# Kernel tuning notes

Measured on AMD Instinct MI355X. Metric: run time of the kernel, lower is better.

## Reference

```python
import jax, jax.numpy as jnp
import numpy as np

B, N, E, H, FF = 8, 1024, 512, 8, 2048
D = E // H
SCALE = D ** -0.5
EPS = 1e-5


def _layernorm(x, g, b):
    mu = jnp.mean(x, axis=-1, keepdims=True)
    var = jnp.mean((x - mu) ** 2, axis=-1, keepdims=True)
    return (x - mu) * jax.lax.rsqrt(var + EPS) * g + b


def setup_inputs() -> dict:
    key = jax.random.key(0)
    ks = jax.random.split(key, 16)
    s = lambda fan_in: 1.0 / np.sqrt(fan_in)
    inp = {"x": jax.random.normal(ks[0], (B, N, E), jnp.float32)}
    # attention projections, stored as [in, out] so y = x @ W + b
    inp["Wq"] = jax.random.uniform(ks[1], (E, E), jnp.float32, -s(E), s(E))
    inp["bq"] = jnp.zeros((E,), jnp.float32)
    inp["Wk"] = jax.random.uniform(ks[2], (E, E), jnp.float32, -s(E), s(E))
    inp["bk"] = jnp.zeros((E,), jnp.float32)
    inp["Wv"] = jax.random.uniform(ks[3], (E, E), jnp.float32, -s(E), s(E))
    inp["bv"] = jnp.zeros((E,), jnp.float32)
    inp["Wo"] = jax.random.uniform(ks[4], (E, E), jnp.float32, -s(E), s(E))
    inp["bo"] = jnp.zeros((E,), jnp.float32)
    # layernorms
    inp["g1"] = jnp.ones((E,), jnp.float32)
    inp["b1"] = jnp.zeros((E,), jnp.float32)
    inp["g2"] = jnp.ones((E,), jnp.float32)
    inp["b2"] = jnp.zeros((E,), jnp.float32)
    # feed-forward
    inp["W1"] = jax.random.uniform(ks[5], (E, FF), jnp.float32, -s(E), s(E))
    inp["bf1"] = jnp.zeros((FF,), jnp.float32)
    inp["W2"] = jax.random.uniform(ks[6], (FF, E), jnp.float32, -s(FF), s(FF))
    inp["bf2"] = jnp.zeros((E,), jnp.float32)
    return inp


def reference(x, Wq, bq, Wk, bk, Wv, bv, Wo, bo, g1, b1, g2, b2, W1, bf1, W2, bf2):
    # --- multi-head self-attention (equivalent to the edge scatter-softmax:
    # softmax over all source nodes j for each target node i) ---
    q = (x @ Wq + bq).reshape(B, N, H, D)
    k = (x @ Wk + bk).reshape(B, N, H, D)
    v = (x @ Wv + bv).reshape(B, N, H, D)
    scores = jnp.einsum("bnhd,bmhd->bhnm", q, k) * SCALE  # [B,H,N,N]
    attn = jax.nn.softmax(scores, axis=-1)
    ctx = jnp.einsum("bhnm,bmhd->bnhd", attn, v).reshape(B, N, E)
    attn_out = ctx @ Wo + bo
    # --- residual + norm1 ---
    h1 = _layernorm(x + attn_out, g1, b1)
    # --- FFN: linear -> relu -> linear ---
    ffn = jax.nn.relu(h1 @ W1 + bf1) @ W2 + bf2
    # --- residual + norm2 ---
    return _layernorm(h1 + ffn, g2, b2)
```

## Files before the change

### kernel.cpp

```cpp
#include <hip/hip_runtime.h>
#include <cstdint>
#include <cstddef>

typedef unsigned short u16;
typedef __attribute__((ext_vector_type(8))) short bf16x8;
typedef __attribute__((ext_vector_type(4))) float f32x4;
typedef __attribute__((ext_vector_type(16))) float f32x16;

#define EPI_F32 0
#define EPI_BF16_RELU 1
#define EPI_QKV 2

#define QSCALE 0.18033688011112042f

__device__ __forceinline__ u16 f2bf(float f) {
  uint32_t u = __float_as_uint(f);
  return (u16)((u + 0x7FFFu + ((u >> 16) & 1u)) >> 16);
}

__device__ __forceinline__ uint32_t cvt_pk_bf16(float lo, float hi) {
  uint32_t r;
  asm("v_cvt_pk_bf16_f32 %0, %1, %2" : "=v"(r) : "v"(lo), "v"(hi));
  return r;
}

__device__ __forceinline__ float fexp2(float x) { return __builtin_amdgcn_exp2f(x); }

__device__ __forceinline__ void gload_lds16(const void* g, void* l) {
  __builtin_amdgcn_global_load_lds((const __attribute__((address_space(1))) void*)g,
                                   (__attribute__((address_space(3))) void*)l, 16, 0, 0);
}

__global__ __launch_bounds__(256) void cvt_kernel(const float* __restrict__ in,
                                                  u16* __restrict__ out, int n8) {
  const int i = blockIdx.x * 256 + threadIdx.x;
  if (i >= n8) return;
  const float4* p = (const float4*)in + (size_t)i * 2;
  float4 a = p[0], b = p[1];
  union { u16 u[8]; uint4 q; } pk;
  pk.u[0] = f2bf(a.x); pk.u[1] = f2bf(a.y); pk.u[2] = f2bf(a.z); pk.u[3] = f2bf(a.w);
  pk.u[4] = f2bf(b.x); pk.u[5] = f2bf(b.y); pk.u[6] = f2bf(b.z); pk.u[7] = f2bf(b.w);
  ((uint4*)out)[i] = pk.q;
}

__global__ __launch_bounds__(256) void tcvt_kernel(const float* __restrict__ W,
                                                   u16* __restrict__ Wt, int K, int N) {
  __shared__ float tl[32][33];
  const int t = threadIdx.x;
  const int kr0 = blockIdx.y * 32, nc0 = blockIdx.x * 32;
  const int r = t >> 3, cq = (t & 7) * 4;
  float4 v = *(const float4*)&W[(size_t)(kr0 + r) * N + nc0 + cq];
  tl[r][cq + 0] = v.x; tl[r][cq + 1] = v.y; tl[r][cq + 2] = v.z; tl[r][cq + 3] = v.w;
  __syncthreads();
  union { u16 u[4]; uint2 q; } pk;
#pragma unroll
  for (int j = 0; j < 4; ++j) pk.u[j] = f2bf(tl[cq + j][r]);
  *(uint2*)&Wt[(size_t)(nc0 + r) * K + kr0 + cq] = pk.q;
}

__global__ __launch_bounds__(256) void packb_kernel(const float* __restrict__ bq,
                                                    const float* __restrict__ bk,
                                                    const float* __restrict__ bv,
                                                    float* __restrict__ out) {
  const int i = blockIdx.x * 256 + threadIdx.x;
  if (i >= 1536) return;
  out[i] = i < 512 ? bq[i] : (i < 1024 ? bk[i - 512] : bv[i - 1024]);
}

template<int BM, int BN, int WM, int WN, int EPI>
__global__ __launch_bounds__(256) void gemm_kernel(
    const u16* __restrict__ A, const u16* __restrict__ Bt,
    const float* __restrict__ bias, void* __restrict__ out,
    int M, int N, int K) {
  constexpr int NWN = BN / WN;
  constexpr int MI = WM / 16, NI = WN / 16;
  __shared__ u16 As[BM * 32];
  __shared__ u16 Bs[BN * 32];
  const int tid = threadIdx.x;
  const int lane = tid & 63;
  const int wave = tid >> 6;
  const int m0 = blockIdx.y * BM;
  const int n0 = blockIdx.x * BN;
  const int wm = wave / NWN, wn = wave % NWN;
  const int g = lane >> 4, lr = lane & 15;
  const int srow = lane >> 2, scol = (lane & 3) * 8;

  f32x4 acc[MI][NI] = {};

  for (int k0 = 0; k0 < K; k0 += 32) {
#pragma unroll
    for (int ch = wave; ch < BM / 16; ch += 4)
      gload_lds16(A + (size_t)(m0 + ch * 16 + srow) * K + k0 + scol, &As[ch * 512]);
#pragma unroll
    for (int ch = wave; ch < BN / 16; ch += 4)
      gload_lds16(Bt + (size_t)(n0 + ch * 16 + srow) * K + k0 + scol, &Bs[ch * 512]);
    __syncthreads();
    bf16x8 a[MI], b[NI];
#pragma unroll
    for (int mi = 0; mi < MI; ++mi) a[mi] = *(const bf16x8*)&As[(wm * WM + mi * 16 + lr) * 32 + g * 8];
#pragma unroll
    for (int ni = 0; ni < NI; ++ni) b[ni] = *(const bf16x8*)&Bs[(wn * WN + ni * 16 + lr) * 32 + g * 8];
#pragma unroll
    for (int mi = 0; mi < MI; ++mi)
#pragma unroll
      for (int ni = 0; ni < NI; ++ni)
        acc[mi][ni] = __builtin_amdgcn_mfma_f32_16x16x32_bf16(a[mi], b[ni], acc[mi][ni], 0, 0, 0);
    __syncthreads();
  }

#pragma unroll
  for (int mi = 0; mi < MI; ++mi) {
#pragma unroll
    for (int ni = 0; ni < NI; ++ni) {
      const int col = n0 + wn * WN + ni * 16 + lr;
      const float bv = bias[col];
      f32x4 v = acc[mi][ni];
#pragma unroll
      for (int r = 0; r < 4; ++r) {
        const int row = m0 + wm * WM + mi * 16 + g * 4 + r;
        const float y = v[r] + bv;
        if (EPI == EPI_F32) {
          ((float*)out)[(size_t)row * N + col] = y;
        } else if (EPI == EPI_BF16_RELU) {
          ((u16*)out)[(size_t)row * N + col] = f2bf(fmaxf(y, 0.f));
        } else {
          u16* qb = (u16*)out;
          const int sec = col >> 9, cs = col & 511;
          const int b = row >> 10, t = row & 1023, h = cs >> 6, d = cs & 63;
          if (sec == 0)
            qb[((size_t)((b * 8 + h) * 1024 + t)) * 64 + d] = f2bf(y * QSCALE);
          else if (sec == 1)
            qb[4194304 + ((size_t)((b * 8 + h) * 1024 + t)) * 64 + d] = f2bf(y);
          else
            qb[8388608 + ((size_t)((b * 8 + h) * 64 + d)) * 1024 + t] = f2bf(y);
        }
      }
    }
  }
}

__global__ __launch_bounds__(256, 2) void attn3_kernel(
    const u16* __restrict__ Q, const u16* __restrict__ K,
    const u16* __restrict__ Vt, u16* __restrict__ ctx) {
  __shared__ u16 tl[4 * 2048];
  const int tid = threadIdx.x, lane = tid & 63, w = tid >> 6;
  const int bh = blockIdx.x >> 3, qb = blockIdx.x & 7;
  const int c = lane & 31, g = lane >> 5;
  const int q0 = qb * 128 + w * 32;

  const u16* Qp = Q + ((size_t)bh * 1024 + q0 + c) * 64 + g * 8;
  const bf16x8 qf0 = *(const bf16x8*)(Qp);
  const bf16x8 qf1 = *(const bf16x8*)(Qp + 16);
  const bf16x8 qf2 = *(const bf16x8*)(Qp + 32);
  const bf16x8 qf3 = *(const bf16x8*)(Qp + 48);

  const u16* Kbase = K + (size_t)bh * 65536;
  const u16* Vbase = Vt + (size_t)bh * 65536;

  f32x16 cacc[2] = {};
  float mrun = -1e30f, lrun = 0.f;

  const u16* Kp0 = Kbase + (size_t)c * 64 + g * 8;
  bf16x8 kf0 = *(const bf16x8*)(Kp0);
  bf16x8 kf1 = *(const bf16x8*)(Kp0 + 16);
  bf16x8 kf2 = *(const bf16x8*)(Kp0 + 32);
  bf16x8 kf3 = *(const bf16x8*)(Kp0 + 48);
  bf16x8 kf4 = *(const bf16x8*)(Kp0 + 2048);
  bf16x8 kf5 = *(const bf16x8*)(Kp0 + 2048 + 16);
  bf16x8 kf6 = *(const bf16x8*)(Kp0 + 2048 + 32);
  bf16x8 kf7 = *(const bf16x8*)(Kp0 + 2048 + 48);

  for (int kt = 0; kt < 16; ++kt) {
    const int key0 = kt * 64;
    const int keyn = ((kt + 1) & 15) * 64;
    const u16* Vp = Vbase + (size_t)c * 1024 + key0 + g * 8;
    const bf16x8 va00 = *(const bf16x8*)(Vp);
    const bf16x8 va01 = *(const bf16x8*)(Vp + 16);
    const bf16x8 va10 = *(const bf16x8*)(Vp + 32768);
    const bf16x8 va11 = *(const bf16x8*)(Vp + 32768 + 16);
    const bf16x8 vb00 = *(const bf16x8*)(Vp + 32);
    const bf16x8 vb01 = *(const bf16x8*)(Vp + 48);
    const bf16x8 vb10 = *(const bf16x8*)(Vp + 32768 + 32);
    const bf16x8 vb11 = *(const bf16x8*)(Vp + 32768 + 48);
    const u16* Kpn = Kbase + (size_t)(keyn + c) * 64 + g * 8;
    const bf16x8 n0 = *(const bf16x8*)(Kpn);
    const bf16x8 n1 = *(const bf16x8*)(Kpn + 16);
    const bf16x8 n2 = *(const bf16x8*)(Kpn + 32);
    const bf16x8 n3 = *(const bf16x8*)(Kpn + 48);
    const bf16x8 n4 = *(const bf16x8*)(Kpn + 2048);
    const bf16x8 n5 = *(const bf16x8*)(Kpn + 2048 + 16);
    const bf16x8 n6 = *(const bf16x8*)(Kpn + 2048 + 32);
    const bf16x8 n7 = *(const bf16x8*)(Kpn + 2048 + 48);

    f32x16 sa = {}, sb = {};
    sa = __builtin_amdgcn_mfma_f32_32x32x16_bf16(kf0, qf0, sa, 0, 0, 0);
    sb = __builtin_amdgcn_mfma_f32_32x32x16_bf16(kf4, qf0, sb, 0, 0, 0);
    sa = __builtin_amdgcn_mfma_f32_32x32x16_bf16(kf1, qf1, sa, 0, 0, 0);
    sb = __builtin_amdgcn_mfma_f32_32x32x16_bf16(kf5, qf1, sb, 0, 0, 0);
    sa = __builtin_amdgcn_mfma_f32_32x32x16_bf16(kf2, qf2, sa, 0, 0, 0);
    sb = __builtin_amdgcn_mfma_f32_32x32x16_bf16(kf6, qf2, sb, 0, 0, 0);
    sa = __builtin_amdgcn_mfma_f32_32x32x16_bf16(kf3, qf3, sa, 0, 0, 0);
    sb = __builtin_amdgcn_mfma_f32_32x32x16_bf16(kf7, qf3, sb, 0, 0, 0);

    float tm[16];
#pragma unroll
    for (int r = 0; r < 16; ++r) tm[r] = fmaxf(sa[r], sb[r]);
#pragma unroll
    for (int st = 8; st >= 1; st >>= 1)
#pragma unroll
      for (int r = 0; r < st; ++r) tm[r] = fmaxf(tm[r], tm[r + st]);
    const float mt = fmaxf(tm[0], __shfl_xor(tm[0], 32));
    if (!__all(mt <= mrun)) {
      const float mnew = fmaxf(mrun, mt);
      const float al = fexp2(mrun - mnew);
#pragma unroll
      for (int r = 0; r < 16; ++r) { cacc[0][r] *= al; cacc[1][r] *= al; }
      lrun *= al;
      mrun = mnew;
    }
    float pa[16], pb[16];
#pragma unroll
    for (int r = 0; r < 16; ++r) pa[r] = fexp2(sa[r] - mrun);
#pragma unroll
    for (int r = 0; r < 16; ++r) pb[r] = fexp2(sb[r] - mrun);
    float ts[16];
#pragma unroll
    for (int r = 0; r < 16; ++r) ts[r] = pa[r] + pb[r];
#pragma unroll
    for (int st = 8; st >= 1; st >>= 1)
#pragma unroll
      for (int r = 0; r < st; ++r) ts[r] += ts[r + st];
    lrun += ts[0] + __shfl_xor(ts[0], 32);

    uint32_t wda[8], pwa[8], wdb[8], pwb[8];
#pragma unroll
    for (int i = 0; i < 8; ++i) wda[i] = cvt_pk_bf16(pa[2 * i], pa[2 * i + 1]);
#pragma unroll
    for (int i = 0; i < 8; ++i) wdb[i] = cvt_pk_bf16(pb[2 * i], pb[2 * i + 1]);
#pragma unroll
    for (int i = 0; i < 8; ++i) pwa[i] = __shfl_xor((int)wda[i], 32);
#pragma unroll
    for (int i = 0; i < 8; ++i) pwb[i] = __shfl_xor((int)wdb[i], 32);
    union { uint32_t u[4]; bf16x8 v; } b0a, b1a, b0b, b1b;
    const bool glo = (g == 0);
    b0a.u[0] = glo ? wda[0] : pwa[2]; b0a.u[1] = glo ? wda[1] : pwa[3];
    b0a.u[2] = glo ? pwa[0] : wda[2]; b0a.u[3] = glo ? pwa[1] : wda[3];
    b1a.u[0] = glo ? wda[4] : pwa[6]; b1a.u[1] = glo ? wda[5] : pwa[7];
    b1a.u[2] = glo ? pwa[4] : wda[6]; b1a.u[3] = glo ? pwa[5] : wda[7];
    b0b.u[0] = glo ? wdb[0] : pwb[2]; b0b.u[1] = glo ? wdb[1] : pwb[3];
    b0b.u[2] = glo ? pwb[0] : wdb[2]; b0b.u[3] = glo ? pwb[1] : wdb[3];
    b1b.u[0] = glo ? wdb[4] : pwb[6]; b1b.u[1] = glo ? wdb[5] : pwb[7];
    b1b.u[2] = glo ? pwb[4] : wdb[6]; b1b.u[3] = glo ? pwb[5] : wdb[7];

    cacc[0] = __builtin_amdgcn_mfma_f32_32x32x16_bf16(va00, b0a.v, cacc[0], 0, 0, 0);
    cacc[1] = __builtin_amdgcn_mfma_f32_32x32x16_bf16(va10, b0a.v, cacc[1], 0, 0, 0);
    cacc[0] = __builtin_amdgcn_mfma_f32_32x32x16_bf16(va01, b1a.v, cacc[0], 0, 0, 0);
    cacc[1] = __builtin_amdgcn_mfma_f32_32x32x16_bf16(va11, b1a.v, cacc[1], 0, 0, 0);
    cacc[0] = __builtin_amdgcn_mfma_f32_32x32x16_bf16(vb00, b0b.v, cacc[0], 0, 0, 0);
    cacc[1] = __builtin_amdgcn_mfma_f32_32x32x16_bf16(vb10, b0b.v, cacc[1], 0, 0, 0);
    cacc[0] = __builtin_amdgcn_mfma_f32_32x32x16_bf16(vb01, b1b.v, cacc[0], 0, 0, 0);
    cacc[1] = __builtin_amdgcn_mfma_f32_32x32x16_bf16(vb11, b1b.v, cacc[1], 0, 0, 0);

    kf0 = n0; kf1 = n1; kf2 = n2; kf3 = n3;
    kf4 = n4; kf5 = n5; kf6 = n6; kf7 = n7;
  }

  const float inv = 1.0f / lrun;
  u16* tw = &tl[w * 2048];
#pragma unroll
  for (int h2 = 0; h2 < 2; ++h2) {
#pragma unroll
    for (int rq = 0; rq < 4; ++rq) {
      const u16 x0 = f2bf(cacc[h2][4 * rq + 0] * inv);
      const u16 x1 = f2bf(cacc[h2][4 * rq + 1] * inv);
      const u16 x2 = f2bf(cacc[h2][4 * rq + 2] * inv);
      const u16 x3 = f2bf(cacc[h2][4 * rq + 3] * inv);
      uint2 val;
      val.x = (uint32_t)x0 | ((uint32_t)x1 << 16);
      val.y = (uint32_t)x2 | ((uint32_t)x3 << 16);
      const int chunk = h2 * 4 + rq;
      *(uint2*)&tw[c * 64 + ((chunk ^ (c & 7)) * 8) + 4 * g] = val;
    }
  }
  __syncthreads();
  const int b_ = bh >> 3, h_ = bh & 7;
#pragma unroll
  for (int t = 0; t < 4; ++t) {
    const int lcg = t * 256 + tid;
    const int wv = lcg >> 8, rem = lcg & 255;
    const int q = rem >> 3, cg = rem & 7;
    const uint4 val = *(const uint4*)&tl[wv * 2048 + q * 64 + ((cg ^ (q & 7)) * 8)];
    const int grow = qb * 128 + wv * 32 + q;
    *(uint4*)&ctx[((size_t)(b_ * 1024 + grow)) * 512 + h_ * 64 + cg * 8] = val;
  }
}

__global__ __launch_bounds__(256) void ln_kernel(
    const float* __restrict__ A, const float* __restrict__ R,
    const float* __restrict__ gw, const float* __restrict__ bw,
    float* __restrict__ outF, u16* __restrict__ outB) {
  const int lane = threadIdx.x & 63, wave = threadIdx.x >> 6;
  const int row = blockIdx.x * 4 + wave;
  const float4* a4 = (const float4*)(A + (size_t)row * 512);
  const float4* r4 = (const float4*)(R + (size_t)row * 512);
  float4 x0 = a4[lane * 2], x1 = a4[lane * 2 + 1];
  float4 y0 = r4[lane * 2], y1 = r4[lane * 2 + 1];
  float v[8] = {x0.x + y0.x, x0.y + y0.y, x0.z + y0.z, x0.w + y0.w,
                x1.x + y1.x, x1.y + y1.y, x1.z + y1.z, x1.w + y1.w};
  float s = 0.f;
#pragma unroll
  for (int j = 0; j < 8; ++j) s += v[j];
#pragma unroll
  for (int off = 32; off >= 1; off >>= 1) s += __shfl_xor(s, off);
  const float mu = s * (1.f / 512.f);
  float vs = 0.f;
#pragma unroll
  for (int j = 0; j < 8; ++j) { const float d = v[j] - mu; vs += d * d; }
#pragma unroll
  for (int off = 32; off >= 1; off >>= 1) vs += __shfl_xor(vs, off);
  const float rstd = rsqrtf(vs * (1.f / 512.f) + 1e-5f);
  float4 gA = ((const float4*)gw)[lane * 2], gB = ((const float4*)gw)[lane * 2 + 1];
  float4 bA = ((const float4*)bw)[lane * 2], bB = ((const float4*)bw)[lane * 2 + 1];
  const float og[8] = {gA.x, gA.y, gA.z, gA.w, gB.x, gB.y, gB.z, gB.w};
  const float ob[8] = {bA.x, bA.y, bA.z, bA.w, bB.x, bB.y, bB.z, bB.w};
  float o[8];
#pragma unroll
  for (int j = 0; j < 8; ++j) o[j] = (v[j] - mu) * rstd * og[j] + ob[j];
  float4 w0 = {o[0], o[1], o[2], o[3]}, w1 = {o[4], o[5], o[6], o[7]};
  ((float4*)(outF + (size_t)row * 512))[lane * 2] = w0;
  ((float4*)(outF + (size_t)row * 512))[lane * 2 + 1] = w1;
  if (outB) {
    union { u16 u[8]; uint4 q; } pk;
#pragma unroll
    for (int j = 0; j < 8; ++j) pk.u[j] = f2bf(o[j]);
    ((uint4*)(outB + (size_t)row * 512))[lane] = pk.q;
  }
}

extern "C" void kernel_launch(void* const* d_in, const int* in_sizes, int n_in,
                              void* d_out, int out_size, void* d_ws, size_t ws_size,
                              hipStream_t stream) {
  const float* x   = (const float*)d_in[0];
  const float* Wq  = (const float*)d_in[1];
  const float* bq  = (const float*)d_in[2];
  const float* Wk  = (const float*)d_in[3];
  const float* bk  = (const float*)d_in[4];
  const float* Wv  = (const float*)d_in[5];
  const float* bv  = (const float*)d_in[6];
  const float* Wo  = (const float*)d_in[7];
  const float* bo  = (const float*)d_in[8];
  const float* g1  = (const float*)d_in[9];
  const float* b1  = (const float*)d_in[10];
  const float* g2  = (const float*)d_in[11];
  const float* b2  = (const float*)d_in[12];
  const float* W1  = (const float*)d_in[13];
  const float* bf1 = (const float*)d_in[14];
  const float* W2  = (const float*)d_in[15];
  const float* bf2 = (const float*)d_in[16];

  char* ws = (char*)d_ws;
  u16*   xb      = (u16*)(ws + 0);
  u16*   Wqkvt   = (u16*)(ws + 8388608);
  u16*   Wot     = (u16*)(ws + 9961472);
  u16*   W1t     = (u16*)(ws + 10485760);
  u16*   W2t     = (u16*)(ws + 12582912);
  u16*   Qb      = (u16*)(ws + 14680064);
  u16*   ctx     = (u16*)(ws + 39845888);
  float* attnout = (float*)(ws + 48234496);
  float* bqkv    = (float*)(ws + 48234496);
  float* h1f     = (float*)(ws + 65011712);
  u16*   h1b     = (u16*)(ws + 81788928);
  u16*   mid     = (u16*)(ws + 31457280);

  cvt_kernel<<<2048, 256, 0, stream>>>(x, xb, 524288);
  tcvt_kernel<<<dim3(16, 16), 256, 0, stream>>>(Wq, Wqkvt, 512, 512);
  tcvt_kernel<<<dim3(16, 16), 256, 0, stream>>>(Wk, Wqkvt + 262144, 512, 512);
  tcvt_kernel<<<dim3(16, 16), 256, 0, stream>>>(Wv, Wqkvt + 524288, 512, 512);
  tcvt_kernel<<<dim3(16, 16), 256, 0, stream>>>(Wo, Wot, 512, 512);
  tcvt_kernel<<<dim3(64, 16), 256, 0, stream>>>(W1, W1t, 512, 2048);
  tcvt_kernel<<<dim3(16, 64), 256, 0, stream>>>(W2, W2t, 2048, 512);
  packb_kernel<<<6, 256, 0, stream>>>(bq, bk, bv, bqkv);

  gemm_kernel<128, 128, 64, 64, EPI_QKV><<<dim3(12, 64), 256, 0, stream>>>(
      xb, Wqkvt, bqkv, Qb, 8192, 1536, 512);

  attn3_kernel<<<512, 256, 0, stream>>>(Qb, Qb + 4194304, Qb + 8388608, ctx);

  gemm_kernel<64, 128, 64, 32, EPI_F32><<<dim3(4, 128), 256, 0, stream>>>(
      ctx, Wot, bo, attnout, 8192, 512, 512);
  ln_kernel<<<2048, 256, 0, stream>>>(x, attnout, g1, b1, h1f, h1b);

  gemm_kernel<128, 128, 64, 64, EPI_BF16_RELU><<<dim3(16, 64), 256, 0, stream>>>(
      h1b, W1t, bf1, mid, 8192, 2048, 512);
  gemm_kernel<64, 128, 64, 32, EPI_F32><<<dim3(4, 128), 256, 0, stream>>>(
      mid, W2t, bf2, (float*)d_out, 8192, 512, 2048);
  ln_kernel<<<2048, 256, 0, stream>>>(h1f, (const float*)d_out, g2, b2, (float*)d_out, nullptr);
}
```

Measured before the change: 320.0 us.

## Split-K output GEMMs with LN-fused reduction, LDS-staged attention, merged weight transposes

The attention kernel now double-buffers K and V tiles into swizzled LDS through global_load_lds instead of reading fragments straight from global memory into registers. The two N=512 GEMMs (Wo and W2) use a 2-way split-K that writes fp32 partials, and the layernorm kernels sum the partials, add the bias and the residual. The second residual now reads the bf16 h1 copy instead of a stored fp32 h1. The four square weight transposes are merged into one launch. The split-K doubles the block count for the narrow GEMMs at the cost of extra partial traffic, and using bf16 h1 as the residual lowers precision slightly.

```diff
diff --git a/kernel.cpp b/kernel.cpp
--- a/kernel.cpp
+++ b/kernel.cpp
@@ -10,6 +10,7 @@
 #define EPI_F32 0
 #define EPI_BF16_RELU 1
 #define EPI_QKV 2
+#define EPI_PART 3
 
 #define QSCALE 0.18033688011112042f
 
@@ -58,6 +59,26 @@
   *(uint2*)&Wt[(size_t)(nc0 + r) * K + kr0 + cq] = pk.q;
 }
 
+__global__ __launch_bounds__(256) void tcvt4_kernel(
+    const float* __restrict__ Wq, const float* __restrict__ Wk,
+    const float* __restrict__ Wv, const float* __restrict__ Wo,
+    u16* __restrict__ outQKV, u16* __restrict__ outO) {
+  __shared__ float tl[32][33];
+  const int z = blockIdx.z;
+  const float* W = z == 0 ? Wq : (z == 1 ? Wk : (z == 2 ? Wv : Wo));
+  u16* Wt = z < 3 ? outQKV + z * 262144 : outO;
+  const int t = threadIdx.x;
+  const int kr0 = blockIdx.y * 32, nc0 = blockIdx.x * 32;
+  const int r = t >> 3, cq = (t & 7) * 4;
+  float4 v = *(const float4*)&W[(size_t)(kr0 + r) * 512 + nc0 + cq];
+  tl[r][cq + 0] = v.x; tl[r][cq + 1] = v.y; tl[r][cq + 2] = v.z; tl[r][cq + 3] = v.w;
+  __syncthreads();
+  union { u16 u[4]; uint2 q; } pk;
+#pragma unroll
+  for (int j = 0; j < 4; ++j) pk.u[j] = f2bf(tl[cq + j][r]);
+  *(uint2*)&Wt[(size_t)(nc0 + r) * 512 + kr0 + cq] = pk.q;
+}
+
 __global__ __launch_bounds__(256) void packb_kernel(const float* __restrict__ bq,
                                                     const float* __restrict__ bk,
                                                     const float* __restrict__ bv,
@@ -67,7 +88,7 @@
   out[i] = i < 512 ? bq[i] : (i < 1024 ? bk[i - 512] : bv[i - 1024]);
 }
 
-template<int BM, int BN, int WM, int WN, int EPI>
+template<int BM, int BN, int WM, int WN, int EPI, int SPLIT>
 __global__ __launch_bounds__(256) void gemm_kernel(
     const u16* __restrict__ A, const u16* __restrict__ Bt,
     const float* __restrict__ bias, void* __restrict__ out,
@@ -87,7 +108,9 @@
 
   f32x4 acc[MI][NI] = {};
 
-  for (int k0 = 0; k0 < K; k0 += 32) {
+  const int kBeg = (SPLIT > 1) ? blockIdx.z * (K / SPLIT) : 0;
+  const int kEnd = (SPLIT > 1) ? kBeg + (K / SPLIT) : K;
+  for (int k0 = kBeg; k0 < kEnd; k0 += 32) {
 #pragma unroll
     for (int ch = wave; ch < BM / 16; ch += 4)
       gload_lds16(A + (size_t)(m0 + ch * 16 + srow) * K + k0 + scol, &As[ch * 512]);
@@ -113,7 +136,7 @@
 #pragma unroll
     for (int ni = 0; ni < NI; ++ni) {
       const int col = n0 + wn * WN + ni * 16 + lr;
-      const float bv = bias[col];
+      const float bv = (EPI == EPI_PART) ? 0.f : bias[col];
       f32x4 v = acc[mi][ni];
 #pragma unroll
       for (int r = 0; r < 4; ++r) {
@@ -121,6 +144,8 @@
         const float y = v[r] + bv;
         if (EPI == EPI_F32) {
           ((float*)out)[(size_t)row * N + col] = y;
+        } else if (EPI == EPI_PART) {
+          ((float*)out)[(size_t)blockIdx.z * M * N + (size_t)row * N + col] = y;
         } else if (EPI == EPI_BF16_RELU) {
           ((u16*)out)[(size_t)row * N + col] = f2bf(fmaxf(y, 0.f));
         } else {
@@ -139,10 +164,10 @@
   }
 }
 
-__global__ __launch_bounds__(256, 2) void attn3_kernel(
+__global__ __launch_bounds__(256, 2) void attn4_kernel(
     const u16* __restrict__ Q, const u16* __restrict__ K,
     const u16* __restrict__ Vt, u16* __restrict__ ctx) {
-  __shared__ u16 tl[4 * 2048];
+  __shared__ u16 smem[16384];
   const int tid = threadIdx.x, lane = tid & 63, w = tid >> 6;
   const int bh = blockIdx.x >> 3, qb = blockIdx.x & 7;
   const int c = lane & 31, g = lane >> 5;
@@ -157,40 +182,36 @@
   const u16* Kbase = K + (size_t)bh * 65536;
   const u16* Vbase = Vt + (size_t)bh * 65536;
 
+  const int r0 = w * 16 + (lane >> 3), r1 = r0 + 8;
+  const int cg0 = ((lane & 7) ^ (r0 & 7)) << 3;
+  const int cg1 = ((lane & 7) ^ (r1 & 7)) << 3;
+
+#define STAGE(buf, key0) do {                                                       \
+    gload_lds16(Kbase + (size_t)((key0) + r0) * 64 + cg0, &smem[(buf)*4096 + w*1024]);       \
+    gload_lds16(Kbase + (size_t)((key0) + r1) * 64 + cg1, &smem[(buf)*4096 + w*1024 + 512]); \
+    gload_lds16(Vbase + (size_t)r0 * 1024 + (key0) + cg0, &smem[8192 + (buf)*4096 + w*1024]);\
+    gload_lds16(Vbase + (size_t)r1 * 1024 + (key0) + cg1, &smem[8192 + (buf)*4096 + w*1024 + 512]); \
+  } while (0)
+
+  const int cs = c & 7;
+  const int ro0 = c * 64, ro1 = (32 + c) * 64;
+#define KS(buf, ro, cg) (*(const bf16x8*)&smem[(buf)*4096 + (ro) + ((((cg)) ^ cs) << 3)])
+#define VS(buf, ro, cg) (*(const bf16x8*)&smem[8192 + (buf)*4096 + (ro) + ((((cg)) ^ cs) << 3)])
+
   f32x16 cacc[2] = {};
   float mrun = -1e30f, lrun = 0.f;
 
-  const u16* Kp0 = Kbase + (size_t)c * 64 + g * 8;
-  bf16x8 kf0 = *(const bf16x8*)(Kp0);
-  bf16x8 kf1 = *(const bf16x8*)(Kp0 + 16);
-  bf16x8 kf2 = *(const bf16x8*)(Kp0 + 32);
-  bf16x8 kf3 = *(const bf16x8*)(Kp0 + 48);
-  bf16x8 kf4 = *(const bf16x8*)(Kp0 + 2048);
-  bf16x8 kf5 = *(const bf16x8*)(Kp0 + 2048 + 16);
-  bf16x8 kf6 = *(const bf16x8*)(Kp0 + 2048 + 32);
-  bf16x8 kf7 = *(const bf16x8*)(Kp0 + 2048 + 48);
+  STAGE(0, 0);
+  __syncthreads();
 
   for (int kt = 0; kt < 16; ++kt) {
-    const int key0 = kt * 64;
-    const int keyn = ((kt + 1) & 15) * 64;
-    const u16* Vp = Vbase + (size_t)c * 1024 + key0 + g * 8;
-    const bf16x8 va00 = *(const bf16x8*)(Vp);
-    const bf16x8 va01 = *(const bf16x8*)(Vp + 16);
-    const bf16x8 va10 = *(const bf16x8*)(Vp + 32768);
-    const bf16x8 va11 = *(const bf16x8*)(Vp + 32768 + 16);
-    const bf16x8 vb00 = *(const bf16x8*)(Vp + 32);
-    const bf16x8 vb01 = *(const bf16x8*)(Vp + 48);
-    const bf16x8 vb10 = *(const bf16x8*)(Vp + 32768 + 32);
-    const bf16x8 vb11 = *(const bf16x8*)(Vp + 32768 + 48);
-    const u16* Kpn = Kbase + (size_t)(keyn + c) * 64 + g * 8;
-    const bf16x8 n0 = *(const bf16x8*)(Kpn);
-    const bf16x8 n1 = *(const bf16x8*)(Kpn + 16);
-    const bf16x8 n2 = *(const bf16x8*)(Kpn + 32);
-    const bf16x8 n3 = *(const bf16x8*)(Kpn + 48);
-    const bf16x8 n4 = *(const bf16x8*)(Kpn + 2048);
-    const bf16x8 n5 = *(const bf16x8*)(Kpn + 2048 + 16);
-    const bf16x8 n6 = *(const bf16x8*)(Kpn + 2048 + 32);
-    const bf16x8 n7 = *(const bf16x8*)(Kpn + 2048 + 48);
+    const int buf = kt & 1;
+    if (kt < 15) STAGE(buf ^ 1, (kt + 1) * 64);
+
+    const bf16x8 kf0 = KS(buf, ro0, g),     kf1 = KS(buf, ro0, 2 + g);
+    const bf16x8 kf2 = KS(buf, ro0, 4 + g), kf3 = KS(buf, ro0, 6 + g);
+    const bf16x8 kf4 = KS(buf, ro1, g),     kf5 = KS(buf, ro1, 2 + g);
+    const bf16x8 kf6 = KS(buf, ro1, 4 + g), kf7 = KS(buf, ro1, 6 + g);
 
     f32x16 sa = {}, sb = {};
     sa = __builtin_amdgcn_mfma_f32_32x32x16_bf16(kf0, qf0, sa, 0, 0, 0);
@@ -252,6 +273,11 @@
     b1b.u[0] = glo ? wdb[4] : pwb[6]; b1b.u[1] = glo ? wdb[5] : pwb[7];
     b1b.u[2] = glo ? pwb[4] : wdb[6]; b1b.u[3] = glo ? pwb[5] : wdb[7];
 
+    const bf16x8 va00 = VS(buf, ro0, g),     va01 = VS(buf, ro0, 2 + g);
+    const bf16x8 vb00 = VS(buf, ro0, 4 + g), vb01 = VS(buf, ro0, 6 + g);
+    const bf16x8 va10 = VS(buf, ro1, g),     va11 = VS(buf, ro1, 2 + g);
+    const bf16x8 vb10 = VS(buf, ro1, 4 + g), vb11 = VS(buf, ro1, 6 + g);
+
     cacc[0] = __builtin_amdgcn_mfma_f32_32x32x16_bf16(va00, b0a.v, cacc[0], 0, 0, 0);
     cacc[1] = __builtin_amdgcn_mfma_f32_32x32x16_bf16(va10, b0a.v, cacc[1], 0, 0, 0);
     cacc[0] = __builtin_amdgcn_mfma_f32_32x32x16_bf16(va01, b1a.v, cacc[0], 0, 0, 0);
@@ -261,12 +287,11 @@
     cacc[0] = __builtin_amdgcn_mfma_f32_32x32x16_bf16(vb01, b1b.v, cacc[0], 0, 0, 0);
     cacc[1] = __builtin_amdgcn_mfma_f32_32x32x16_bf16(vb11, b1b.v, cacc[1], 0, 0, 0);
 
-    kf0 = n0; kf1 = n1; kf2 = n2; kf3 = n3;
-    kf4 = n4; kf5 = n5; kf6 = n6; kf7 = n7;
+    __syncthreads();
   }
 
   const float inv = 1.0f / lrun;
-  u16* tw = &tl[w * 2048];
+  u16* tw = &smem[w * 2048];
 #pragma unroll
   for (int h2 = 0; h2 < 2; ++h2) {
 #pragma unroll
@@ -289,24 +314,44 @@
     const int lcg = t * 256 + tid;
     const int wv = lcg >> 8, rem = lcg & 255;
     const int q = rem >> 3, cg = rem & 7;
-    const uint4 val = *(const uint4*)&tl[wv * 2048 + q * 64 + ((cg ^ (q & 7)) * 8)];
+    const uint4 val = *(const uint4*)&smem[wv * 2048 + q * 64 + ((cg ^ (q & 7)) * 8)];
     const int grow = qb * 128 + wv * 32 + q;
     *(uint4*)&ctx[((size_t)(b_ * 1024 + grow)) * 512 + h_ * 64 + cg * 8] = val;
   }
-}
-
-__global__ __launch_bounds__(256) void ln_kernel(
-    const float* __restrict__ A, const float* __restrict__ R,
+#undef STAGE
+#undef KS
+#undef VS
+}
+
+template<bool ABF16>
+__global__ __launch_bounds__(256) void lnc_kernel(
+    const void* __restrict__ Av, const float* __restrict__ P0,
+    const float* __restrict__ P1, const float* __restrict__ pb,
     const float* __restrict__ gw, const float* __restrict__ bw,
     float* __restrict__ outF, u16* __restrict__ outB) {
   const int lane = threadIdx.x & 63, wave = threadIdx.x >> 6;
   const int row = blockIdx.x * 4 + wave;
-  const float4* a4 = (const float4*)(A + (size_t)row * 512);
-  const float4* r4 = (const float4*)(R + (size_t)row * 512);
-  float4 x0 = a4[lane * 2], x1 = a4[lane * 2 + 1];
-  float4 y0 = r4[lane * 2], y1 = r4[lane * 2 + 1];
-  float v[8] = {x0.x + y0.x, x0.y + y0.y, x0.z + y0.z, x0.w + y0.w,
-                x1.x + y1.x, x1.y + y1.y, x1.z + y1.z, x1.w + y1.w};
+  float a[8];
+  if (ABF16) {
+    const uint4 q = ((const uint4*)((const u16*)Av + (size_t)row * 512))[lane];
+    const u16* pu = (const u16*)&q;
+#pragma unroll
+    for (int j = 0; j < 8; ++j) a[j] = __uint_as_float((uint32_t)pu[j] << 16);
+  } else {
+    const float4* a4 = (const float4*)((const float*)Av + (size_t)row * 512);
+    const float4 x0 = a4[lane * 2], x1 = a4[lane * 2 + 1];
+    a[0] = x0.x; a[1] = x0.y; a[2] = x0.z; a[3] = x0.w;
+    a[4] = x1.x; a[5] = x1.y; a[6] = x1.z; a[7] = x1.w;
+  }
+  const float4* p04 = (const float4*)(P0 + (size_t)row * 512);
+  const float4* p14 = (const float4*)(P1 + (size_t)row * 512);
+  const float4 q00 = p04[lane * 2], q01 = p04[lane * 2 + 1];
+  const float4 q10 = p14[lane * 2], q11 = p14[lane * 2 + 1];
+  const float4 e0 = ((const float4*)pb)[lane * 2], e1 = ((const float4*)pb)[lane * 2 + 1];
+  float v[8] = {a[0] + q00.x + q10.x + e0.x, a[1] + q00.y + q10.y + e0.y,
+                a[2] + q00.z + q10.z + e0.z, a[3] + q00.w + q10.w + e0.w,
+                a[4] + q01.x + q11.x + e1.x, a[5] + q01.y + q11.y + e1.y,
+                a[6] + q01.z + q11.z + e1.z, a[7] + q01.w + q11.w + e1.w};
   float s = 0.f;
 #pragma unroll
   for (int j = 0; j < 8; ++j) s += v[j];
@@ -319,16 +364,18 @@
 #pragma unroll
   for (int off = 32; off >= 1; off >>= 1) vs += __shfl_xor(vs, off);
   const float rstd = rsqrtf(vs * (1.f / 512.f) + 1e-5f);
-  float4 gA = ((const float4*)gw)[lane * 2], gB = ((const float4*)gw)[lane * 2 + 1];
-  float4 bA = ((const float4*)bw)[lane * 2], bB = ((const float4*)bw)[lane * 2 + 1];
+  const float4 gA = ((const float4*)gw)[lane * 2], gB = ((const float4*)gw)[lane * 2 + 1];
+  const float4 bA = ((const float4*)bw)[lane * 2], bB = ((const float4*)bw)[lane * 2 + 1];
   const float og[8] = {gA.x, gA.y, gA.z, gA.w, gB.x, gB.y, gB.z, gB.w};
   const float ob[8] = {bA.x, bA.y, bA.z, bA.w, bB.x, bB.y, bB.z, bB.w};
   float o[8];
 #pragma unroll
   for (int j = 0; j < 8; ++j) o[j] = (v[j] - mu) * rstd * og[j] + ob[j];
-  float4 w0 = {o[0], o[1], o[2], o[3]}, w1 = {o[4], o[5], o[6], o[7]};
-  ((float4*)(outF + (size_t)row * 512))[lane * 2] = w0;
-  ((float4*)(outF + (size_t)row * 512))[lane * 2 + 1] = w1;
+  if (outF) {
+    float4 w0 = {o[0], o[1], o[2], o[3]}, w1 = {o[4], o[5], o[6], o[7]};
+    ((float4*)(outF + (size_t)row * 512))[lane * 2] = w0;
+    ((float4*)(outF + (size_t)row * 512))[lane * 2 + 1] = w1;
+  }
   if (outB) {
     union { u16 u[8]; uint4 q; } pk;
 #pragma unroll
@@ -359,40 +406,39 @@
   const float* bf2 = (const float*)d_in[16];
 
   char* ws = (char*)d_ws;
-  u16*   xb      = (u16*)(ws + 0);
-  u16*   Wqkvt   = (u16*)(ws + 8388608);
-  u16*   Wot     = (u16*)(ws + 9961472);
-  u16*   W1t     = (u16*)(ws + 10485760);
-  u16*   W2t     = (u16*)(ws + 12582912);
-  u16*   Qb      = (u16*)(ws + 14680064);
-  u16*   ctx     = (u16*)(ws + 39845888);
-  float* attnout = (float*)(ws + 48234496);
-  float* bqkv    = (float*)(ws + 48234496);
-  float* h1f     = (float*)(ws + 65011712);
-  u16*   h1b     = (u16*)(ws + 81788928);
-  u16*   mid     = (u16*)(ws + 31457280);
+  u16*   xb    = (u16*)(ws + 0);
+  u16*   Wqkvt = (u16*)(ws + 8388608);
+  u16*   Wot   = (u16*)(ws + 9961472);
+  u16*   W1t   = (u16*)(ws + 10485760);
+  u16*   W2t   = (u16*)(ws + 12582912);
+  u16*   Qb    = (u16*)(ws + 14680064);
+  u16*   ctx   = (u16*)(ws + 39845888);
+  float* P0    = (float*)(ws + 48234496);
+  u16*   h1b   = (u16*)(ws + 81788928);
+  u16*   mid   = (u16*)(ws + 14680064);
+  float* bqkv  = (float*)(ws + 39845888);
 
   cvt_kernel<<<2048, 256, 0, stream>>>(x, xb, 524288);
-  tcvt_kernel<<<dim3(16, 16), 256, 0, stream>>>(Wq, Wqkvt, 512, 512);
-  tcvt_kernel<<<dim3(16, 16), 256, 0, stream>>>(Wk, Wqkvt + 262144, 512, 512);
-  tcvt_kernel<<<dim3(16, 16), 256, 0, stream>>>(Wv, Wqkvt + 524288, 512, 512);
-  tcvt_kernel<<<dim3(16, 16), 256, 0, stream>>>(Wo, Wot, 512, 512);
+  tcvt4_kernel<<<dim3(16, 16, 4), 256, 0, stream>>>(Wq, Wk, Wv, Wo, Wqkvt, Wot);
   tcvt_kernel<<<dim3(64, 16), 256, 0, stream>>>(W1, W1t, 512, 2048);
   tcvt_kernel<<<dim3(16, 64), 256, 0, stream>>>(W2, W2t, 2048, 512);
   packb_kernel<<<6, 256, 0, stream>>>(bq, bk, bv, bqkv);
 
-  gemm_kernel<128, 128, 64, 64, EPI_QKV><<<dim3(12, 64), 256, 0, stream>>>(
+  gemm_kernel<128, 128, 64, 64, EPI_QKV, 1><<<dim3(12, 64), 256, 0, stream>>>(
       xb, Wqkvt, bqkv, Qb, 8192, 1536, 512);
 
-  attn3_kernel<<<512, 256, 0, stream>>>(Qb, Qb + 4194304, Qb + 8388608, ctx);
-
-  gemm_kernel<64, 128, 64, 32, EPI_F32><<<dim3(4, 128), 256, 0, stream>>>(
-      ctx, Wot, bo, attnout, 8192, 512, 512);
-  ln_kernel<<<2048, 256, 0, stream>>>(x, attnout, g1, b1, h1f, h1b);
-
-  gemm_kernel<128, 128, 64, 64, EPI_BF16_RELU><<<dim3(16, 64), 256, 0, stream>>>(
+  attn4_kernel<<<512, 256, 0, stream>>>(Qb, Qb + 4194304, Qb + 8388608, ctx);
+
+  gemm_kernel<64, 128, 64, 32, EPI_PART, 2><<<dim3(4, 128, 2), 256, 0, stream>>>(
+      ctx, Wot, nullptr, P0, 8192, 512, 512);
+  lnc_kernel<false><<<2048, 256, 0, stream>>>(x, P0, P0 + 4194304, bo, g1, b1,
+                                              nullptr, h1b);
+
+  gemm_kernel<128, 128, 64, 64, EPI_BF16_RELU, 1><<<dim3(16, 64), 256, 0, stream>>>(
       h1b, W1t, bf1, mid, 8192, 2048, 512);
-  gemm_kernel<64, 128, 64, 32, EPI_F32><<<dim3(4, 128), 256, 0, stream>>>(
-      mid, W2t, bf2, (float*)d_out, 8192, 512, 2048);
-  ln_kernel<<<2048, 256, 0, stream>>>(h1f, (const float*)d_out, g2, b2, (float*)d_out, nullptr);
-}
+
+  gemm_kernel<64, 128, 64, 32, EPI_PART, 2><<<dim3(4, 128, 2), 256, 0, stream>>>(
+      mid, W2t, nullptr, P0, 8192, 512, 2048);
+  lnc_kernel<true><<<2048, 256, 0, stream>>>(h1b, P0, P0 + 4194304, bf2, g2, b2,
+                                             (float*)d_out, nullptr);
+}
```

New measurement: 270.2 us. 15.6% less time.
